# Optimization experiments

Measured on AMD Instinct MI355X. Metric: run time of the kernel, lower is better.

## Reference

```python
import jax, jax.numpy as jnp
import numpy as np

GRID = 512
F_FEAT = 32
CORE = 16
N_PTS = 2097152
SCALE = 0.1


def _bilinear_sample(plane, coords):
    """plane: (F, H, W); coords: (N, 2) with (x, y) in [-1, 1], align_corners=True.
    Returns (F, N)."""
    F_, H, W = plane.shape
    x = (coords[:, 0] + 1.0) * 0.5 * (W - 1)
    y = (coords[:, 1] + 1.0) * 0.5 * (H - 1)
    x0f = jnp.floor(x)
    y0f = jnp.floor(y)
    wx = x - x0f  # (N,)
    wy = y - y0f
    x0 = jnp.clip(x0f.astype(jnp.int32), 0, W - 1)
    x1 = jnp.clip(x0 + 1, 0, W - 1)
    y0 = jnp.clip(y0f.astype(jnp.int32), 0, H - 1)
    y1 = jnp.clip(y0 + 1, 0, H - 1)
    v00 = plane[:, y0, x0]  # (F, N)
    v01 = plane[:, y0, x1]
    v10 = plane[:, y1, x0]
    v11 = plane[:, y1, x1]
    return (v00 * (1.0 - wx) * (1.0 - wy)
            + v01 * wx * (1.0 - wy)
            + v10 * (1.0 - wx) * wy
            + v11 * wx * wy)


def setup_inputs() -> dict:
    key = jax.random.key(0)
    k1, k2, k3, k4, k5 = jax.random.split(key, 5)
    coords_plane = jax.random.uniform(
        k1, (3, 1, N_PTS, 1, 2), dtype=jnp.float32, minval=-1.0, maxval=1.0)
    plane_xy = SCALE * jax.random.normal(k2, (1, F_FEAT, GRID, GRID), dtype=jnp.float32)
    plane_yz = SCALE * jax.random.normal(k3, (1, F_FEAT, GRID, GRID), dtype=jnp.float32)
    plane_xz = SCALE * jax.random.normal(k4, (1, F_FEAT, GRID, GRID), dtype=jnp.float32)
    core_tensor = jax.random.normal(k5, (CORE, F_FEAT), dtype=jnp.float32)
    return {"coords_plane": coords_plane, "plane_xy": plane_xy,
            "plane_yz": plane_yz, "plane_xz": plane_xz,
            "core_tensor": core_tensor}


def reference(coords_plane, plane_xy, plane_yz, plane_xz, core_tensor):
    # coords_plane: (3, 1, N, 1, 2) -> (3, N, 2)
    c = coords_plane.reshape(3, -1, 2)
    f_xy = _bilinear_sample(plane_xy[0], c[0])  # (F, N)
    f_yz = _bilinear_sample(plane_yz[0], c[1])
    f_xz = _bilinear_sample(plane_xz[0], c[2])
    prod = f_xy * f_yz * f_xz                   # (F, N)
    # sum over core dim: out[f, n] = (sum_k core[k, f]) * prod[f, n]
    scale = jnp.sum(core_tensor, axis=0)        # (F,)
    out = (scale[:, None] * prod).T             # (N, F)
    return out
```

## Files before the change

### kernel.cpp

```cpp
#include <hip/hip_runtime.h>
#include <hip/hip_fp16.h>

#define N_PTS 2097152
#define GRID_ 512
#define F_FEAT 32
#define HW (GRID_ * GRID_)
#define HWF ((size_t)HW * F_FEAT)

#define NBINS 64
#define BIN_SHIFT 3
#define BIN_CAP 36864
#define CUR_STRIDE 32
#define PTS_PER_BLOCK 2048
#define SLOTS_PER_BLOCK 256
#define BPB 144
#define FULL_SUB 100

typedef float f32x4 __attribute__((ext_vector_type(4)));
typedef unsigned long long u64;

__global__ void td_scale_kernel(const float* __restrict__ core,
                                float* __restrict__ scale) {
    int f = threadIdx.x;
    float s = 0.0f;
#pragma unroll
    for (int k = 0; k < 16; ++k) s += core[k * F_FEAT + f];
    scale[f] = s;
}

__global__ void td_transpose_kernel(const float* __restrict__ pxy,
                                    const float* __restrict__ pyz,
                                    const float* __restrict__ pxz,
                                    const float* __restrict__ scale,
                                    __half* __restrict__ wsh) {
    __shared__ float tile[32][33];
    const int plane = blockIdx.z;
    const float* src = (plane == 0) ? pxy : ((plane == 1) ? pyz : pxz);
    __half* dst = wsh + (size_t)plane * HWF;
    const int y = blockIdx.y;
    const int x0 = blockIdx.x * 32;
    const int tx = threadIdx.x;

    for (int i = threadIdx.y; i < 32; i += 8) {
        tile[i][tx] = src[(size_t)i * HW + (size_t)y * GRID_ + x0 + tx];
    }
    __syncthreads();
    const int h = tx & 15;
    const int xo = tx >> 4;
    float sc0 = 1.0f, sc1 = 1.0f;
    if (plane == 0) {
        sc0 = scale[2 * h];
        sc1 = scale[2 * h + 1];
    }
    __half2* dst2 = reinterpret_cast<__half2*>(dst);
    for (int i2 = threadIdx.y; i2 < 16; i2 += 8) {
        const int i = i2 * 2 + xo;
        const float a = tile[2 * h][i] * sc0;
        const float b = tile[2 * h + 1][i] * sc1;
        dst2[((size_t)(y * GRID_ + x0 + i)) * 16 + h] = __floats2half2_rn(a, b);
    }
}

__global__ void td_zero_kernel(int* __restrict__ cursor) {
    for (int i = threadIdx.x; i < 3 * NBINS * CUR_STRIDE; i += 256) cursor[i] = 0;
}

__global__ __launch_bounds__(256) void td_bin_kernel(
    const float2* __restrict__ coords, int* __restrict__ cursor,
    u64* __restrict__ recs) {
    __shared__ int lhist[NBINS];
    __shared__ int lposx[NBINS + 1];
    __shared__ int lbase[NBINS];
    __shared__ u64 lsorted[PTS_PER_BLOCK];
    const int pl = blockIdx.y;
    const int tid = threadIdx.x;
    const int base_p = blockIdx.x * PTS_PER_BLOCK;
    if (tid < NBINS) lhist[tid] = 0;
    __syncthreads();

    u64 myrec[8];
    int mybin[8], myslot[8];
#pragma unroll
    for (int k = 0; k < 8; ++k) {
        const int p = base_p + k * 256 + tid;
        const float2 c = coords[(size_t)pl * N_PTS + p];
        const float xf = (c.x + 1.0f) * 0.5f * (float)(GRID_ - 1);
        const float yf = (c.y + 1.0f) * 0.5f * (float)(GRID_ - 1);
        const float x0f = floorf(xf);
        const float y0f = floorf(yf);
        const float wx = xf - x0f;
        const float wy = yf - y0f;
        int x0 = min(max((int)x0f, 0), GRID_ - 1);
        int y0 = min(max((int)y0f, 0), GRID_ - 1);
        const int qwx = min(4095, (int)(wx * 4096.0f + 0.5f));
        const int qwy = min(4095, (int)(wy * 4096.0f + 0.5f));
        const int bin = y0 >> BIN_SHIFT;
        myrec[k] = (u64)p | ((u64)x0 << 21) | ((u64)y0 << 30) |
                   ((u64)qwx << 39) | ((u64)qwy << 51);
        mybin[k] = bin;
        myslot[k] = atomicAdd(&lhist[bin], 1);
    }
    __syncthreads();

    if (tid < 64) {
        const int cnt = lhist[tid];
        int v = cnt;
#pragma unroll
        for (int o = 1; o < 64; o <<= 1) {
            const int t = __shfl_up(v, o, 64);
            if (tid >= o) v += t;
        }
        lposx[tid] = v - cnt;
        if (tid == 63) lposx[64] = v;
        lbase[tid] =
            (cnt > 0)
                ? atomicAdd(&cursor[(pl * NBINS + tid) * CUR_STRIDE], cnt)
                : 0;
    }
    __syncthreads();

#pragma unroll
    for (int k = 0; k < 8; ++k) lsorted[lposx[mybin[k]] + myslot[k]] = myrec[k];
    __syncthreads();

#pragma unroll
    for (int r = 0; r < 8; ++r) {
        const int s = r * 256 + tid;
        int lo = 0, hi = 64;
        while (hi - lo > 1) {
            const int mid = (lo + hi) >> 1;
            if (lposx[mid] <= s) lo = mid;
            else hi = mid;
        }
        const int gslot = lbase[lo] + (s - lposx[lo]);
        if (gslot < BIN_CAP)
            recs[((size_t)pl * NBINS + lo) * BIN_CAP + gslot] = lsorted[s];
    }
}

__device__ __forceinline__ int td_bin_of_block(int i, int* sub) {
    const int xcd = i & 7;
    const int j = i >> 3;
    const int g = j / BPB;
    *sub = j - g * BPB;
    return g * 8 + xcd;
}

__global__ __launch_bounds__(256) void td_sample_binned_kernel(
    const u64* __restrict__ recs, const int* __restrict__ cursor,
    const f32x4* __restrict__ ws4, f32x4* __restrict__ feat) {
    __shared__ u64 srecs[SLOTS_PER_BLOCK];
    const int pl = blockIdx.y;
    int sub;
    const int bin = td_bin_of_block(blockIdx.x, &sub);
    const int tid = threadIdx.x;
    const int fq = tid & 3;
    const int q = tid >> 2;
    const int sbase = sub * SLOTS_PER_BLOCK;
    const bool full = (sub < FULL_SUB);
    int cnt = sbase + SLOTS_PER_BLOCK;
    if (!full) {
        cnt = min(cursor[(pl * NBINS + bin) * CUR_STRIDE], BIN_CAP);
        if (sbase >= cnt) return;
    }

    const size_t rbase = ((size_t)pl * NBINS + bin) * BIN_CAP;
    srecs[tid] = recs[rbase + (full ? (sbase + tid) : min(sbase + tid, cnt - 1))];
    __syncthreads();

    const f32x4* tp = ws4 + (size_t)pl * (HWF / 8);

    u64 r[4];
    bool act[4];
#pragma unroll
    for (int t = 0; t < 4; ++t) {
        const int ls = q + t * 64;
        act[t] = full | ((sbase + ls) < cnt);
        r[t] = srecs[act[t] ? ls : 0];
    }

    int pid[4];
    size_t idx[4][4];
    float w[4][4];
#pragma unroll
    for (int t = 0; t < 4; ++t) {
        pid[t] = (int)(r[t] & 0x1FFFFF);
        const int x0 = (int)((r[t] >> 21) & 511);
        const int y0 = (int)((r[t] >> 30) & 511);
        const float wx = (float)((int)((r[t] >> 39) & 4095)) * (1.0f / 4096.0f);
        const float wy = (float)((int)((r[t] >> 51) & 4095)) * (1.0f / 4096.0f);
        const int x1 = min(x0 + 1, GRID_ - 1);
        const int y1 = min(y0 + 1, GRID_ - 1);
        idx[t][0] = (size_t)(y0 * GRID_ + x0) * 4 + fq;
        idx[t][1] = (size_t)(y0 * GRID_ + x1) * 4 + fq;
        idx[t][2] = (size_t)(y1 * GRID_ + x0) * 4 + fq;
        idx[t][3] = (size_t)(y1 * GRID_ + x1) * 4 + fq;
        w[t][0] = (1.0f - wx) * (1.0f - wy);
        w[t][1] = wx * (1.0f - wy);
        w[t][2] = (1.0f - wx) * wy;
        w[t][3] = wx * wy;
    }

    f32x4 v[4][4];
#pragma unroll
    for (int t = 0; t < 4; ++t)
#pragma unroll
        for (int c = 0; c < 4; ++c) v[t][c] = tp[idx[t][c]];

#pragma unroll
    for (int t = 0; t < 4; ++t) {
        if (!act[t]) continue;
        const half2* h0 = reinterpret_cast<const half2*>(&v[t][0]);
        const half2* h1 = reinterpret_cast<const half2*>(&v[t][1]);
        const half2* h2 = reinterpret_cast<const half2*>(&v[t][2]);
        const half2* h3 = reinterpret_cast<const half2*>(&v[t][3]);
        union {
            f32x4 vv;
            half2 h[4];
        } u;
#pragma unroll
        for (int j = 0; j < 4; ++j) {
            const float2 f00 = __half22float2(h0[j]);
            const float2 f01 = __half22float2(h1[j]);
            const float2 f10 = __half22float2(h2[j]);
            const float2 f11 = __half22float2(h3[j]);
            const float sa = f00.x * w[t][0] + f01.x * w[t][1] +
                             f10.x * w[t][2] + f11.x * w[t][3];
            const float sb = f00.y * w[t][0] + f01.y * w[t][1] +
                             f10.y * w[t][2] + f11.y * w[t][3];
            u.h[j] = __floats2half2_rn(sa, sb);
        }
        __builtin_nontemporal_store(u.vv,
                                    &feat[(size_t)pid[t] * 12 + pl * 4 + fq]);
    }
}

__global__ __launch_bounds__(256) void td_combine_stream_kernel(
    const f32x4* __restrict__ feat, f32x4* __restrict__ out) {
    const size_t t = (size_t)blockIdx.x * 256 + threadIdx.x;
    const size_t pid = t >> 2;
    const int fq = (int)(t & 3);

    union U {
        f32x4 v;
        half2 h[4];
    };
    U a, b, c;
    a.v = __builtin_nontemporal_load(&feat[pid * 12 + fq]);
    b.v = __builtin_nontemporal_load(&feat[pid * 12 + 4 + fq]);
    c.v = __builtin_nontemporal_load(&feat[pid * 12 + 8 + fq]);

    float rr[8];
#pragma unroll
    for (int j = 0; j < 4; ++j) {
        const float2 fa = __half22float2(a.h[j]);
        const float2 fb = __half22float2(b.h[j]);
        const float2 fc = __half22float2(c.h[j]);
        rr[2 * j] = fa.x * fb.x * fc.x;
        rr[2 * j + 1] = fa.y * fb.y * fc.y;
    }
    f32x4 o0, o1;
    o0.x = rr[0]; o0.y = rr[1]; o0.z = rr[2]; o0.w = rr[3];
    o1.x = rr[4]; o1.y = rr[5]; o1.z = rr[6]; o1.w = rr[7];
    __builtin_nontemporal_store(o0, &out[pid * 8 + fq * 2]);
    __builtin_nontemporal_store(o1, &out[pid * 8 + fq * 2 + 1]);
}

__global__ __launch_bounds__(256) void td_sample_kernel(
    const float2* __restrict__ coords, const f32x4* __restrict__ ws4,
    f32x4* __restrict__ out) {
    const int tid = blockIdx.x * 256 + threadIdx.x;
    const int p = tid >> 2;
    const int fq = tid & 3;

    const float2 c0 = coords[p];
    const float2 c1 = coords[N_PTS + p];
    const float2 c2 = coords[2 * N_PTS + p];

    size_t idx[3][4];
    float w[3][4];
    const float2 cc[3] = {c0, c1, c2};
#pragma unroll
    for (int pl = 0; pl < 3; ++pl) {
        const float xf = (cc[pl].x + 1.0f) * 0.5f * (float)(GRID_ - 1);
        const float yf = (cc[pl].y + 1.0f) * 0.5f * (float)(GRID_ - 1);
        const float x0f = floorf(xf);
        const float y0f = floorf(yf);
        const float wx = xf - x0f;
        const float wy = yf - y0f;
        int x0 = min(max((int)x0f, 0), GRID_ - 1);
        int y0 = min(max((int)y0f, 0), GRID_ - 1);
        const int x1 = min(x0 + 1, GRID_ - 1);
        const int y1 = min(y0 + 1, GRID_ - 1);
        const size_t base = (size_t)pl * (HWF / 8);
        idx[pl][0] = base + (size_t)(y0 * GRID_ + x0) * 4 + fq;
        idx[pl][1] = base + (size_t)(y0 * GRID_ + x1) * 4 + fq;
        idx[pl][2] = base + (size_t)(y1 * GRID_ + x0) * 4 + fq;
        idx[pl][3] = base + (size_t)(y1 * GRID_ + x1) * 4 + fq;
        w[pl][0] = (1.0f - wx) * (1.0f - wy);
        w[pl][1] = wx * (1.0f - wy);
        w[pl][2] = (1.0f - wx) * wy;
        w[pl][3] = wx * wy;
    }

    f32x4 v[3][4];
#pragma unroll
    for (int pl = 0; pl < 3; ++pl)
#pragma unroll
        for (int cnr = 0; cnr < 4; ++cnr) v[pl][cnr] = ws4[idx[pl][cnr]];

    float prod[8];
#pragma unroll
    for (int j = 0; j < 8; ++j) prod[j] = 1.0f;
#pragma unroll
    for (int pl = 0; pl < 3; ++pl) {
        const half2* h0 = reinterpret_cast<const half2*>(&v[pl][0]);
        const half2* h1 = reinterpret_cast<const half2*>(&v[pl][1]);
        const half2* h2 = reinterpret_cast<const half2*>(&v[pl][2]);
        const half2* h3 = reinterpret_cast<const half2*>(&v[pl][3]);
#pragma unroll
        for (int j = 0; j < 4; ++j) {
            const float2 f00 = __half22float2(h0[j]);
            const float2 f01 = __half22float2(h1[j]);
            const float2 f10 = __half22float2(h2[j]);
            const float2 f11 = __half22float2(h3[j]);
            prod[2 * j] *= f00.x * w[pl][0] + f01.x * w[pl][1] +
                           f10.x * w[pl][2] + f11.x * w[pl][3];
            prod[2 * j + 1] *= f00.y * w[pl][0] + f01.y * w[pl][1] +
                               f10.y * w[pl][2] + f11.y * w[pl][3];
        }
    }

    f32x4 o0, o1;
    o0.x = prod[0]; o0.y = prod[1]; o0.z = prod[2]; o0.w = prod[3];
    o1.x = prod[4]; o1.y = prod[5]; o1.z = prod[6]; o1.w = prod[7];
    __builtin_nontemporal_store(o0, &out[(size_t)tid * 2]);
    __builtin_nontemporal_store(o1, &out[(size_t)tid * 2 + 1]);
}

__global__ __launch_bounds__(256) void td_fallback_kernel(
    const float* __restrict__ coords, const float* __restrict__ pxy,
    const float* __restrict__ pyz, const float* __restrict__ pxz,
    const float* __restrict__ core, float* __restrict__ out) {
    const int tid = blockIdx.x * 256 + threadIdx.x;
    const int p = tid >> 5;
    const int f = tid & 31;

    float s = 0.0f;
#pragma unroll
    for (int k = 0; k < 16; ++k) s += core[k * F_FEAT + f];

    float prod = s;
    const float* planes[3] = {pxy, pyz, pxz};
#pragma unroll
    for (int plane = 0; plane < 3; ++plane) {
        const float cx = coords[((size_t)plane * N_PTS + p) * 2 + 0];
        const float cy = coords[((size_t)plane * N_PTS + p) * 2 + 1];
        const float xf = (cx + 1.0f) * 0.5f * (float)(GRID_ - 1);
        const float yf = (cy + 1.0f) * 0.5f * (float)(GRID_ - 1);
        const float x0f = floorf(xf);
        const float y0f = floorf(yf);
        const float wx = xf - x0f;
        const float wy = yf - y0f;
        int x0 = min(max((int)x0f, 0), GRID_ - 1);
        int y0 = min(max((int)y0f, 0), GRID_ - 1);
        const int x1 = min(x0 + 1, GRID_ - 1);
        const int y1 = min(y0 + 1, GRID_ - 1);
        const float* src = planes[plane] + (size_t)f * HW;
        const float v00 = src[y0 * GRID_ + x0];
        const float v01 = src[y0 * GRID_ + x1];
        const float v10 = src[y1 * GRID_ + x0];
        const float v11 = src[y1 * GRID_ + x1];
        prod *= v00 * (1.0f - wx) * (1.0f - wy) + v01 * wx * (1.0f - wy) +
                v10 * (1.0f - wx) * wy + v11 * wx * wy;
    }
    out[(size_t)p * F_FEAT + f] = prod;
}

extern "C" void kernel_launch(void* const* d_in, const int* in_sizes, int n_in,
                              void* d_out, int out_size, void* d_ws,
                              size_t ws_size, hipStream_t stream) {
    const float* coords = (const float*)d_in[0];
    const float* pxy = (const float*)d_in[1];
    const float* pyz = (const float*)d_in[2];
    const float* pxz = (const float*)d_in[3];
    const float* core = (const float*)d_in[4];
    float* out = (float*)d_out;

    size_t off = 0;
    auto alloc = [&off](size_t bytes) {
        size_t o = off;
        off = (off + bytes + 255) & ~(size_t)255;
        return o;
    };
    const size_t off_wsh = alloc(3 * HWF * sizeof(__half));
    const size_t off_scale = alloc(32 * sizeof(float));
    const size_t need_r4 = off;
    const size_t off_cur = alloc((size_t)3 * NBINS * CUR_STRIDE * sizeof(int));
    const size_t off_recs = alloc((size_t)3 * NBINS * BIN_CAP * sizeof(u64));
    const size_t off_feat = alloc((size_t)N_PTS * 192);
    const size_t need_full = off;

    char* ws = (char*)d_ws;

    if (ws_size >= need_r4) {
        __half* wsh = (__half*)(ws + off_wsh);
        float* scale = (float*)(ws + off_scale);
        td_scale_kernel<<<1, 32, 0, stream>>>(core, scale);
        td_transpose_kernel<<<dim3(GRID_ / 32, GRID_, 3), dim3(32, 8), 0,
                              stream>>>(pxy, pyz, pxz, scale, wsh);
        if (ws_size >= need_full) {
            int* cursor = (int*)(ws + off_cur);
            u64* recs = (u64*)(ws + off_recs);
            f32x4* feat = (f32x4*)(ws + off_feat);
            td_zero_kernel<<<1, 256, 0, stream>>>(cursor);
            td_bin_kernel<<<dim3(N_PTS / PTS_PER_BLOCK, 3), 256, 0, stream>>>(
                (const float2*)coords, cursor, recs);
            td_sample_binned_kernel<<<dim3(NBINS * BPB, 3), 256, 0, stream>>>(
                recs, cursor, (const f32x4*)wsh, feat);
            td_combine_stream_kernel<<<N_PTS * 4 / 256, 256, 0, stream>>>(
                (const f32x4*)feat, (f32x4*)out);
        } else {
            td_sample_kernel<<<N_PTS * 4 / 256, 256, 0, stream>>>(
                (const float2*)coords, (const f32x4*)wsh, (f32x4*)out);
        }
    } else {
        td_fallback_kernel<<<N_PTS * 32 / 256, 256, 0, stream>>>(
            coords, pxy, pyz, pxz, core, out);
    }
}
```

Baseline: 326.0 us.

## Merge binning, plane transpose and core-sum into one heterogeneous prep kernel

Fuses the scale reduction, plane transpose and point binning into a single launch. Block index selects either a binning role or a transpose role, so the two independent preprocessing jobs run concurrently on the device instead of back to back. Transpose blocks now handle eight rows each, and plane-0 blocks recompute the core sum into shared memory. This removes two launches and the serialization between them, at the cost of redundant core-sum work and possible load imbalance or occupancy limits from the combined shared-memory footprint.

```diff
diff --git a/kernel.cpp b/kernel.cpp
--- a/kernel.cpp
+++ b/kernel.cpp
@@ -16,125 +16,140 @@
 #define BPB 144
 #define FULL_SUB 100
 
+#define BIN_BLOCKS (3 * (N_PTS / PTS_PER_BLOCK))
+#define TR_BLOCKS (3 * 1024)
+
 typedef float f32x4 __attribute__((ext_vector_type(4)));
 typedef unsigned long long u64;
 
-__global__ void td_scale_kernel(const float* __restrict__ core,
-                                float* __restrict__ scale) {
-    int f = threadIdx.x;
-    float s = 0.0f;
-#pragma unroll
-    for (int k = 0; k < 16; ++k) s += core[k * F_FEAT + f];
-    scale[f] = s;
-}
-
-__global__ void td_transpose_kernel(const float* __restrict__ pxy,
-                                    const float* __restrict__ pyz,
-                                    const float* __restrict__ pxz,
-                                    const float* __restrict__ scale,
-                                    __half* __restrict__ wsh) {
-    __shared__ float tile[32][33];
-    const int plane = blockIdx.z;
-    const float* src = (plane == 0) ? pxy : ((plane == 1) ? pyz : pxz);
-    __half* dst = wsh + (size_t)plane * HWF;
-    const int y = blockIdx.y;
-    const int x0 = blockIdx.x * 32;
-    const int tx = threadIdx.x;
-
-    for (int i = threadIdx.y; i < 32; i += 8) {
-        tile[i][tx] = src[(size_t)i * HW + (size_t)y * GRID_ + x0 + tx];
-    }
-    __syncthreads();
-    const int h = tx & 15;
-    const int xo = tx >> 4;
-    float sc0 = 1.0f, sc1 = 1.0f;
-    if (plane == 0) {
-        sc0 = scale[2 * h];
-        sc1 = scale[2 * h + 1];
-    }
-    __half2* dst2 = reinterpret_cast<__half2*>(dst);
-    for (int i2 = threadIdx.y; i2 < 16; i2 += 8) {
-        const int i = i2 * 2 + xo;
-        const float a = tile[2 * h][i] * sc0;
-        const float b = tile[2 * h + 1][i] * sc1;
-        dst2[((size_t)(y * GRID_ + x0 + i)) * 16 + h] = __floats2half2_rn(a, b);
-    }
-}
-
 __global__ void td_zero_kernel(int* __restrict__ cursor) {
     for (int i = threadIdx.x; i < 3 * NBINS * CUR_STRIDE; i += 256) cursor[i] = 0;
 }
 
-__global__ __launch_bounds__(256) void td_bin_kernel(
-    const float2* __restrict__ coords, int* __restrict__ cursor,
-    u64* __restrict__ recs) {
-    __shared__ int lhist[NBINS];
-    __shared__ int lposx[NBINS + 1];
-    __shared__ int lbase[NBINS];
-    __shared__ u64 lsorted[PTS_PER_BLOCK];
-    const int pl = blockIdx.y;
+__global__ __launch_bounds__(256) void td_prep_kernel(
+    const float2* __restrict__ coords, const float* __restrict__ pxy,
+    const float* __restrict__ pyz, const float* __restrict__ pxz,
+    const float* __restrict__ core, int* __restrict__ cursor,
+    u64* __restrict__ recs, __half* __restrict__ wsh) {
+    const int b = blockIdx.x;
     const int tid = threadIdx.x;
-    const int base_p = blockIdx.x * PTS_PER_BLOCK;
-    if (tid < NBINS) lhist[tid] = 0;
-    __syncthreads();
-
-    u64 myrec[8];
-    int mybin[8], myslot[8];
-#pragma unroll
-    for (int k = 0; k < 8; ++k) {
-        const int p = base_p + k * 256 + tid;
-        const float2 c = coords[(size_t)pl * N_PTS + p];
-        const float xf = (c.x + 1.0f) * 0.5f * (float)(GRID_ - 1);
-        const float yf = (c.y + 1.0f) * 0.5f * (float)(GRID_ - 1);
-        const float x0f = floorf(xf);
-        const float y0f = floorf(yf);
-        const float wx = xf - x0f;
-        const float wy = yf - y0f;
-        int x0 = min(max((int)x0f, 0), GRID_ - 1);
-        int y0 = min(max((int)y0f, 0), GRID_ - 1);
-        const int qwx = min(4095, (int)(wx * 4096.0f + 0.5f));
-        const int qwy = min(4095, (int)(wy * 4096.0f + 0.5f));
-        const int bin = y0 >> BIN_SHIFT;
-        myrec[k] = (u64)p | ((u64)x0 << 21) | ((u64)y0 << 30) |
-                   ((u64)qwx << 39) | ((u64)qwy << 51);
-        mybin[k] = bin;
-        myslot[k] = atomicAdd(&lhist[bin], 1);
-    }
-    __syncthreads();
-
-    if (tid < 64) {
-        const int cnt = lhist[tid];
-        int v = cnt;
-#pragma unroll
-        for (int o = 1; o < 64; o <<= 1) {
-            const int t = __shfl_up(v, o, 64);
-            if (tid >= o) v += t;
-        }
-        lposx[tid] = v - cnt;
-        if (tid == 63) lposx[64] = v;
-        lbase[tid] =
-            (cnt > 0)
-                ? atomicAdd(&cursor[(pl * NBINS + tid) * CUR_STRIDE], cnt)
-                : 0;
-    }
-    __syncthreads();
-
-#pragma unroll
-    for (int k = 0; k < 8; ++k) lsorted[lposx[mybin[k]] + myslot[k]] = myrec[k];
-    __syncthreads();
-
-#pragma unroll
-    for (int r = 0; r < 8; ++r) {
-        const int s = r * 256 + tid;
-        int lo = 0, hi = 64;
-        while (hi - lo > 1) {
-            const int mid = (lo + hi) >> 1;
-            if (lposx[mid] <= s) lo = mid;
-            else hi = mid;
-        }
-        const int gslot = lbase[lo] + (s - lposx[lo]);
-        if (gslot < BIN_CAP)
-            recs[((size_t)pl * NBINS + lo) * BIN_CAP + gslot] = lsorted[s];
+
+    if (b < BIN_BLOCKS) {
+        __shared__ int lhist[NBINS];
+        __shared__ int lposx[NBINS + 1];
+        __shared__ int lbase[NBINS];
+        __shared__ u64 lsorted[PTS_PER_BLOCK];
+        const int pl = b >> 10;
+        const int bx = b & 1023;
+        const int base_p = bx * PTS_PER_BLOCK;
+        if (tid < NBINS) lhist[tid] = 0;
+        __syncthreads();
+
+        u64 myrec[8];
+        int mybin[8], myslot[8];
+#pragma unroll
+        for (int k = 0; k < 8; ++k) {
+            const int p = base_p + k * 256 + tid;
+            const float2 c = coords[(size_t)pl * N_PTS + p];
+            const float xf = (c.x + 1.0f) * 0.5f * (float)(GRID_ - 1);
+            const float yf = (c.y + 1.0f) * 0.5f * (float)(GRID_ - 1);
+            const float x0f = floorf(xf);
+            const float y0f = floorf(yf);
+            const float wx = xf - x0f;
+            const float wy = yf - y0f;
+            int x0 = min(max((int)x0f, 0), GRID_ - 1);
+            int y0 = min(max((int)y0f, 0), GRID_ - 1);
+            const int qwx = min(4095, (int)(wx * 4096.0f + 0.5f));
+            const int qwy = min(4095, (int)(wy * 4096.0f + 0.5f));
+            const int bin = y0 >> BIN_SHIFT;
+            myrec[k] = (u64)p | ((u64)x0 << 21) | ((u64)y0 << 30) |
+                       ((u64)qwx << 39) | ((u64)qwy << 51);
+            mybin[k] = bin;
+            myslot[k] = atomicAdd(&lhist[bin], 1);
+        }
+        __syncthreads();
+
+        if (tid < 64) {
+            const int cnt = lhist[tid];
+            int v = cnt;
+#pragma unroll
+            for (int o = 1; o < 64; o <<= 1) {
+                const int t = __shfl_up(v, o, 64);
+                if (tid >= o) v += t;
+            }
+            lposx[tid] = v - cnt;
+            if (tid == 63) lposx[64] = v;
+            lbase[tid] =
+                (cnt > 0)
+                    ? atomicAdd(&cursor[(pl * NBINS + tid) * CUR_STRIDE], cnt)
+                    : 0;
+        }
+        __syncthreads();
+
+#pragma unroll
+        for (int k = 0; k < 8; ++k)
+            lsorted[lposx[mybin[k]] + myslot[k]] = myrec[k];
+        __syncthreads();
+
+#pragma unroll
+        for (int r = 0; r < 8; ++r) {
+            const int s = r * 256 + tid;
+            int lo = 0, hi = 64;
+            while (hi - lo > 1) {
+                const int mid = (lo + hi) >> 1;
+                if (lposx[mid] <= s) lo = mid;
+                else hi = mid;
+            }
+            const int gslot = lbase[lo] + (s - lposx[lo]);
+            if (gslot < BIN_CAP)
+                recs[((size_t)pl * NBINS + lo) * BIN_CAP + gslot] = lsorted[s];
+        }
+    } else {
+        __shared__ float tile[32][33];
+        __shared__ float sscale[32];
+        const int t = b - BIN_BLOCKS;
+        const int plane = t >> 10;
+        const int rr = t & 1023;
+        const int yb = (rr >> 4) << 3;
+        const int x0 = (rr & 15) << 5;
+        const int tx = tid & 31;
+        const int ty = tid >> 5;
+        const float* src = (plane == 0) ? pxy : ((plane == 1) ? pyz : pxz);
+        __half* dst = wsh + (size_t)plane * HWF;
+        __half2* dst2 = reinterpret_cast<__half2*>(dst);
+
+        if (plane == 0 && tid < 32) {
+            float s = 0.0f;
+#pragma unroll
+            for (int k = 0; k < 16; ++k) s += core[k * F_FEAT + tid];
+            sscale[tid] = s;
+        }
+        __syncthreads();
+
+        const int h = tx & 15;
+        const int xo = tx >> 4;
+        float sc0 = 1.0f, sc1 = 1.0f;
+        if (plane == 0) {
+            sc0 = sscale[2 * h];
+            sc1 = sscale[2 * h + 1];
+        }
+
+        for (int yy = 0; yy < 8; ++yy) {
+            const int y = yb + yy;
+            for (int i = ty; i < 32; i += 8) {
+                tile[i][tx] =
+                    src[(size_t)i * HW + (size_t)y * GRID_ + x0 + tx];
+            }
+            __syncthreads();
+            for (int i2 = ty; i2 < 16; i2 += 8) {
+                const int i = i2 * 2 + xo;
+                const float a = tile[2 * h][i] * sc0;
+                const float bb = tile[2 * h + 1][i] * sc1;
+                dst2[((size_t)(y * GRID_ + x0 + i)) * 16 + h] =
+                    __floats2half2_rn(a, bb);
+            }
+            __syncthreads();
+        }
     }
 }
 
@@ -264,6 +279,48 @@
     o1.x = rr[4]; o1.y = rr[5]; o1.z = rr[6]; o1.w = rr[7];
     __builtin_nontemporal_store(o0, &out[pid * 8 + fq * 2]);
     __builtin_nontemporal_store(o1, &out[pid * 8 + fq * 2 + 1]);
+}
+
+__global__ void td_scale_kernel(const float* __restrict__ core,
+                                float* __restrict__ scale) {
+    int f = threadIdx.x;
+    float s = 0.0f;
+#pragma unroll
+    for (int k = 0; k < 16; ++k) s += core[k * F_FEAT + f];
+    scale[f] = s;
+}
+
+__global__ void td_transpose_kernel(const float* __restrict__ pxy,
+                                    const float* __restrict__ pyz,
+                                    const float* __restrict__ pxz,
+                                    const float* __restrict__ scale,
+                                    __half* __restrict__ wsh) {
+    __shared__ float tile[32][33];
+    const int plane = blockIdx.z;
+    const float* src = (plane == 0) ? pxy : ((plane == 1) ? pyz : pxz);
+    __half* dst = wsh + (size_t)plane * HWF;
+    const int y = blockIdx.y;
+    const int x0 = blockIdx.x * 32;
+    const int tx = threadIdx.x;
+
+    for (int i = threadIdx.y; i < 32; i += 8) {
+        tile[i][tx] = src[(size_t)i * HW + (size_t)y * GRID_ + x0 + tx];
+    }
+    __syncthreads();
+    const int h = tx & 15;
+    const int xo = tx >> 4;
+    float sc0 = 1.0f, sc1 = 1.0f;
+    if (plane == 0) {
+        sc0 = scale[2 * h];
+        sc1 = scale[2 * h + 1];
+    }
+    __half2* dst2 = reinterpret_cast<__half2*>(dst);
+    for (int i2 = threadIdx.y; i2 < 16; i2 += 8) {
+        const int i = i2 * 2 + xo;
+        const float a = tile[2 * h][i] * sc0;
+        const float b = tile[2 * h + 1][i] * sc1;
+        dst2[((size_t)(y * GRID_ + x0 + i)) * 16 + h] = __floats2half2_rn(a, b);
+    }
 }
 
 __global__ __launch_bounds__(256) void td_sample_kernel(
@@ -403,27 +460,26 @@
 
     char* ws = (char*)d_ws;
 
-    if (ws_size >= need_r4) {
+    if (ws_size >= need_full) {
+        __half* wsh = (__half*)(ws + off_wsh);
+        int* cursor = (int*)(ws + off_cur);
+        u64* recs = (u64*)(ws + off_recs);
+        f32x4* feat = (f32x4*)(ws + off_feat);
+        td_zero_kernel<<<1, 256, 0, stream>>>(cursor);
+        td_prep_kernel<<<BIN_BLOCKS + TR_BLOCKS, 256, 0, stream>>>(
+            (const float2*)coords, pxy, pyz, pxz, core, cursor, recs, wsh);
+        td_sample_binned_kernel<<<dim3(NBINS * BPB, 3), 256, 0, stream>>>(
+            recs, cursor, (const f32x4*)wsh, feat);
+        td_combine_stream_kernel<<<N_PTS * 4 / 256, 256, 0, stream>>>(
+            (const f32x4*)feat, (f32x4*)out);
+    } else if (ws_size >= need_r4) {
         __half* wsh = (__half*)(ws + off_wsh);
         float* scale = (float*)(ws + off_scale);
         td_scale_kernel<<<1, 32, 0, stream>>>(core, scale);
         td_transpose_kernel<<<dim3(GRID_ / 32, GRID_, 3), dim3(32, 8), 0,
                               stream>>>(pxy, pyz, pxz, scale, wsh);
-        if (ws_size >= need_full) {
-            int* cursor = (int*)(ws + off_cur);
-            u64* recs = (u64*)(ws + off_recs);
-            f32x4* feat = (f32x4*)(ws + off_feat);
-            td_zero_kernel<<<1, 256, 0, stream>>>(cursor);
-            td_bin_kernel<<<dim3(N_PTS / PTS_PER_BLOCK, 3), 256, 0, stream>>>(
-                (const float2*)coords, cursor, recs);
-            td_sample_binned_kernel<<<dim3(NBINS * BPB, 3), 256, 0, stream>>>(
-                recs, cursor, (const f32x4*)wsh, feat);
-            td_combine_stream_kernel<<<N_PTS * 4 / 256, 256, 0, stream>>>(
-                (const f32x4*)feat, (f32x4*)out);
-        } else {
-            td_sample_kernel<<<N_PTS * 4 / 256, 256, 0, stream>>>(
-                (const float2*)coords, (const f32x4*)wsh, (f32x4*)out);
-        }
+        td_sample_kernel<<<N_PTS * 4 / 256, 256, 0, stream>>>(
+            (const float2*)coords, (const f32x4*)wsh, (f32x4*)out);
     } else {
         td_fallback_kernel<<<N_PTS * 32 / 256, 256, 0, stream>>>(
             coords, pxy, pyz, pxz, core, out);
```

New measurement: 319.1 us. 2.1% less time.
